# Kernel tuning notes

Hardware: AMD Instinct MI355X
Metric: run time of the kernel (lower is better)

The kernel has to match this reference:

```python
import jax, jax.numpy as jnp
import numpy as np

B, N, F, O = 4, 4096, 64, 64


def setup_inputs() -> dict:
    key = jax.random.key(0)
    k0, k1, k2, k3, k4 = jax.random.split(key, 5)
    x = jax.random.normal(k0, (B, N, F), dtype=jnp.float32)
    # adj_transform: Linear(2F -> 1): weight (2F,), bias scalar
    adj_w = jax.random.normal(k1, (2 * F,), dtype=jnp.float32) * (1.0 / np.sqrt(2 * F))
    adj_b = jax.random.normal(k2, (), dtype=jnp.float32)
    # GCN weight: xavier_normal_ over (F, O)
    weight = jax.random.normal(k3, (F, O), dtype=jnp.float32) * np.sqrt(2.0 / (F + O))
    bias = jax.random.normal(k4, (O,), dtype=jnp.float32)
    return {"x": x, "adj_w": adj_w, "adj_b": adj_b, "weight": weight, "bias": bias}


def reference(x, adj_w, adj_b, weight, bias):
    f = x.shape[-1]
    # Original: tmp[b,i,j] = x[b,j]; adj[b,i,j] = Linear(cat(x[b,j], x[b,i]))
    # = x[b,j]\u00b7adj_w[:F] + x[b,i]\u00b7adj_w[F:] + adj_b  (exact decomposition,
    # avoids materializing the (B,N,N,2F) concat tensor)
    s_col = jnp.einsum('bnf,f->bn', x, adj_w[:f])   # contributes along j
    s_row = jnp.einsum('bnf,f->bn', x, adj_w[f:])   # contributes along i
    adj = s_row[:, :, None] + s_col[:, None, :] + adj_b  # (B, N, N)
    # symmetric degree normalization with clamp(min=1)
    deg_inv_sqrt = jnp.clip(adj.sum(axis=-1), 1.0, None) ** -0.5  # (B, N)
    adj = deg_inv_sqrt[:, :, None] * adj * deg_inv_sqrt[:, None, :]
    out = jnp.einsum('bij,bjo->bio', adj, x @ weight) + bias
    return jax.nn.relu(out)
```

## Files before the change

### kernel.cpp

```cpp
#include <hip/hip_runtime.h>

#define Bq 4
#define Nq 4096
#define Fq 64
#define Oq 64


__global__ __launch_bounds__(256) void k1_rowdots(
    const float* __restrict__ x, const float* __restrict__ adj_w,
    float* __restrict__ s_row, float* __restrict__ s_col,
    float* __restrict__ blocksum) {
  int r = blockIdx.x * 256 + threadIdx.x;
  const float4* xr = reinterpret_cast<const float4*>(x + (size_t)r * Fq);
  const float4* w0 = reinterpret_cast<const float4*>(adj_w);
  const float4* w1 = reinterpret_cast<const float4*>(adj_w + Fq);
  float sc = 0.f, sr = 0.f;
#pragma unroll
  for (int k = 0; k < Fq / 4; ++k) {
    float4 v = xr[k];
    float4 a = w0[k];
    float4 b = w1[k];
    sc += v.x * a.x + v.y * a.y + v.z * a.z + v.w * a.w;
    sr += v.x * b.x + v.y * b.y + v.z * b.z + v.w * b.w;
  }
  s_col[r] = sc;
  s_row[r] = sr;
  __shared__ float red[256];
  red[threadIdx.x] = sc;
  __syncthreads();
  for (int s = 128; s > 0; s >>= 1) {
    if (threadIdx.x < s) red[threadIdx.x] += red[threadIdx.x + s];
    __syncthreads();
  }
  if (threadIdx.x == 0) blocksum[blockIdx.x] = red[0];
}

__global__ __launch_bounds__(256) void k2_weighted(
    const float* __restrict__ x, const float* __restrict__ s_row,
    const float* __restrict__ s_col, const float* __restrict__ blocksum,
    const float* __restrict__ adj_bp, float* __restrict__ pxd,
    float* __restrict__ pxsd) {
  int b = blockIdx.x >> 5;
  int chunk = blockIdx.x & 31;
  int fq = threadIdx.x & 15;
  int jsub = threadIdx.x >> 4;
  const float adj_b = adj_bp[0];
  float scs = 0.f;
#pragma unroll
  for (int k = 0; k < 16; ++k) scs += blocksum[b * 16 + k];
  const int jcnt = Nq / 32;
  int j0 = chunk * jcnt;
  float4 axd = {0.f, 0.f, 0.f, 0.f};
  float4 axsd = {0.f, 0.f, 0.f, 0.f};
  for (int j = j0 + jsub; j < j0 + jcnt; j += 16) {
    int row = b * Nq + j;
    float srj = s_row[row];
    float scj = s_col[row];
    float dj = rsqrtf(fmaxf(fmaf((float)Nq, srj + adj_b, scs), 1.0f));
    float sdj = scj * dj;
    float4 xv = reinterpret_cast<const float4*>(x + (size_t)row * Fq)[fq];
    axd.x = fmaf(dj, xv.x, axd.x);
    axd.y = fmaf(dj, xv.y, axd.y);
    axd.z = fmaf(dj, xv.z, axd.z);
    axd.w = fmaf(dj, xv.w, axd.w);
    axsd.x = fmaf(sdj, xv.x, axsd.x);
    axsd.y = fmaf(sdj, xv.y, axsd.y);
    axsd.z = fmaf(sdj, xv.z, axsd.z);
    axsd.w = fmaf(sdj, xv.w, axsd.w);
  }
  __shared__ float red[2][16][64];
  *reinterpret_cast<float4*>(&red[0][jsub][fq * 4]) = axd;
  *reinterpret_cast<float4*>(&red[1][jsub][fq * 4]) = axsd;
  __syncthreads();
  int t = threadIdx.x;
  if (t < 64) {
    float s = 0.f;
#pragma unroll
    for (int c = 0; c < 16; ++c) s += red[0][c][t];
    pxd[blockIdx.x * 64 + t] = s;
  } else if (t < 128) {
    int f = t & 63;
    float s = 0.f;
#pragma unroll
    for (int c = 0; c < 16; ++c) s += red[1][c][f];
    pxsd[blockIdx.x * 64 + f] = s;
  }
}

__global__ __launch_bounds__(256) void k3_out(
    const float* __restrict__ s_row, const float* __restrict__ blocksum,
    const float* __restrict__ adj_bp, const float* __restrict__ pxd,
    const float* __restrict__ pxsd, const float* __restrict__ weight,
    const float* __restrict__ bias, float* __restrict__ out) {
  int b = blockIdx.x >> 6;
  int ibase = (blockIdx.x & 63) << 6;
  const float adj_b = adj_bp[0];
  float scs = 0.f;
#pragma unroll
  for (int k = 0; k < 16; ++k) scs += blocksum[b * 16 + k];
  __shared__ float xdl[64], xsdl[64], u[64], v[64];
  int t = threadIdx.x;
  if (t < 128) {
    int f = t & 63;
    const float* p = ((t < 64) ? pxd : pxsd) + (size_t)(b * 32) * 64 + f;
    float a = 0.f;
#pragma unroll
    for (int c = 0; c < 32; ++c) a += p[c * 64];
    if (t < 64)
      xdl[f] = a;
    else
      xsdl[f] = a;
  }
  __syncthreads();
  if (t < 128) {
    int o = t & 63;
    const float* src = (t < 64) ? xdl : xsdl;
    float acc = 0.f;
#pragma unroll
    for (int f = 0; f < Fq; ++f) acc = fmaf(src[f], weight[f * Oq + o], acc);
    if (t < 64)
      u[o] = acc;
    else
      v[o] = acc;
  }
  __syncthreads();
  int o0 = (t & 15) * 4;
#pragma unroll
  for (int pass = 0; pass < 4; ++pass) {
    int row = ibase + pass * 16 + (t >> 4);
    int rg = b * Nq + row;
    float sr = s_row[rg];
    float rowsum = fmaf((float)Nq, sr + adj_b, scs);
    float di = rsqrtf(fmaxf(rowsum, 1.0f));
    float a = di * (sr + adj_b);
    float4 r;
    r.x = fmaxf(0.f, fmaf(a, u[o0 + 0], fmaf(di, v[o0 + 0], bias[o0 + 0])));
    r.y = fmaxf(0.f, fmaf(a, u[o0 + 1], fmaf(di, v[o0 + 1], bias[o0 + 1])));
    r.z = fmaxf(0.f, fmaf(a, u[o0 + 2], fmaf(di, v[o0 + 2], bias[o0 + 2])));
    r.w = fmaxf(0.f, fmaf(a, u[o0 + 3], fmaf(di, v[o0 + 3], bias[o0 + 3])));
    reinterpret_cast<float4*>(out + (size_t)rg * Oq)[t & 15] = r;
  }
}

extern "C" void kernel_launch(void* const* d_in, const int* in_sizes, int n_in,
                              void* d_out, int out_size, void* d_ws,
                              size_t ws_size, hipStream_t stream) {
  const float* x = (const float*)d_in[0];
  const float* adj_w = (const float*)d_in[1];
  const float* adj_b = (const float*)d_in[2];
  const float* weight = (const float*)d_in[3];
  const float* bias = (const float*)d_in[4];
  float* out = (float*)d_out;

  float* ws = (float*)d_ws;
  float* s_row = ws;
  float* s_col = ws + Bq * Nq;
  float* blocksum = ws + 2 * Bq * Nq;
  float* pxd = blocksum + 64;
  float* pxsd = pxd + 128 * 64;

  k1_rowdots<<<64, 256, 0, stream>>>(x, adj_w, s_row, s_col, blocksum);
  k2_weighted<<<Bq * 32, 256, 0, stream>>>(x, s_row, s_col, blocksum, adj_b,
                                           pxd, pxsd);
  k3_out<<<256, 256, 0, stream>>>(s_row, blocksum, adj_b, pxd, pxsd, weight,
                                  bias, out);
}
```

Before: 72.66 us.

## Fuse three kernels into one cooperative kernel with grid syncs

Merges the row-dot, weighted-sum and output kernels into a single cooperative launch of 256 blocks. Each block handles 64 rows and keeps s_row, s_col and degree values in shared memory across phases, with two grid-wide syncs replacing the kernel boundaries. This removes two launch gaps and the global round-trips for per-row scalars. In exchange it depends on all blocks being co-resident and adds the cost of the grid barriers.

```diff
diff --git a/kernel.cpp b/kernel.cpp
--- a/kernel.cpp
+++ b/kernel.cpp
@@ -1,111 +1,125 @@
 #include <hip/hip_runtime.h>
+#include <hip/hip_cooperative_groups.h>
+
+namespace cg = cooperative_groups;
 
 #define Bq 4
 #define Nq 4096
 #define Fq 64
 #define Oq 64
 
+__global__ __launch_bounds__(256) void gcn_fused(
+    const float* __restrict__ x, const float* __restrict__ adj_w,
+    const float* __restrict__ adj_bp, const float* __restrict__ weight,
+    const float* __restrict__ bias, float* __restrict__ out,
+    float* __restrict__ blksum, float* __restrict__ pxd,
+    float* __restrict__ pxsd) {
+  const int t = threadIdx.x;
+  const int blk = blockIdx.x;
+  const int batch = blk >> 6;
+  const float adj_b = adj_bp[0];
 
-__global__ __launch_bounds__(256) void k1_rowdots(
-    const float* __restrict__ x, const float* __restrict__ adj_w,
-    float* __restrict__ s_row, float* __restrict__ s_col,
-    float* __restrict__ blocksum) {
-  int r = blockIdx.x * 256 + threadIdx.x;
-  const float4* xr = reinterpret_cast<const float4*>(x + (size_t)r * Fq);
-  const float4* w0 = reinterpret_cast<const float4*>(adj_w);
-  const float4* w1 = reinterpret_cast<const float4*>(adj_w + Fq);
-  float sc = 0.f, sr = 0.f;
+  __shared__ float ls_row[64], ls_col[64], ld[64], lsd[64];
+  __shared__ float red[2][16][64];
+  __shared__ float xdl[64], xsdl[64], ul[64], vl[64];
+  __shared__ float s_scs;
+
+  {
+    const int g = t >> 2;
+    const int l = t & 3;
+    const int r = blk * 64 + g;
+    const float4* xr = reinterpret_cast<const float4*>(x + (size_t)r * Fq);
+    const float4* w0 = reinterpret_cast<const float4*>(adj_w);
+    const float4* w1 = reinterpret_cast<const float4*>(adj_w + Fq);
+    float sc = 0.f, sr = 0.f;
 #pragma unroll
-  for (int k = 0; k < Fq / 4; ++k) {
-    float4 v = xr[k];
-    float4 a = w0[k];
-    float4 b = w1[k];
-    sc += v.x * a.x + v.y * a.y + v.z * a.z + v.w * a.w;
-    sr += v.x * b.x + v.y * b.y + v.z * b.z + v.w * b.w;
+    for (int k = 0; k < 4; ++k) {
+      const int idx = k * 4 + l;
+      float4 xv = xr[idx];
+      float4 wa = w0[idx];
+      float4 wb = w1[idx];
+      sc += xv.x * wa.x + xv.y * wa.y + xv.z * wa.z + xv.w * wa.w;
+      sr += xv.x * wb.x + xv.y * wb.y + xv.z * wb.z + xv.w * wb.w;
+    }
+    sc += __shfl_xor(sc, 1);
+    sc += __shfl_xor(sc, 2);
+    sr += __shfl_xor(sr, 1);
+    sr += __shfl_xor(sr, 2);
+    if (l == 0) {
+      ls_col[g] = sc;
+      ls_row[g] = sr;
+    }
   }
-  s_col[r] = sc;
-  s_row[r] = sr;
-  __shared__ float red[256];
-  red[threadIdx.x] = sc;
   __syncthreads();
-  for (int s = 128; s > 0; s >>= 1) {
-    if (threadIdx.x < s) red[threadIdx.x] += red[threadIdx.x + s];
-    __syncthreads();
+  if (t < 64) {
+    float val = ls_col[t];
+#pragma unroll
+    for (int m = 1; m < 64; m <<= 1) val += __shfl_xor(val, m);
+    if (t == 0) blksum[blk] = val;
   }
-  if (threadIdx.x == 0) blocksum[blockIdx.x] = red[0];
-}
+  __threadfence();
+  cg::this_grid().sync();
 
-__global__ __launch_bounds__(256) void k2_weighted(
-    const float* __restrict__ x, const float* __restrict__ s_row,
-    const float* __restrict__ s_col, const float* __restrict__ blocksum,
-    const float* __restrict__ adj_bp, float* __restrict__ pxd,
-    float* __restrict__ pxsd) {
-  int b = blockIdx.x >> 5;
-  int chunk = blockIdx.x & 31;
-  int fq = threadIdx.x & 15;
-  int jsub = threadIdx.x >> 4;
-  const float adj_b = adj_bp[0];
-  float scs = 0.f;
+  if (t < 64) {
+    float val = blksum[batch * 64 + t];
 #pragma unroll
-  for (int k = 0; k < 16; ++k) scs += blocksum[b * 16 + k];
-  const int jcnt = Nq / 32;
-  int j0 = chunk * jcnt;
-  float4 axd = {0.f, 0.f, 0.f, 0.f};
-  float4 axsd = {0.f, 0.f, 0.f, 0.f};
-  for (int j = j0 + jsub; j < j0 + jcnt; j += 16) {
-    int row = b * Nq + j;
-    float srj = s_row[row];
-    float scj = s_col[row];
-    float dj = rsqrtf(fmaxf(fmaf((float)Nq, srj + adj_b, scs), 1.0f));
-    float sdj = scj * dj;
-    float4 xv = reinterpret_cast<const float4*>(x + (size_t)row * Fq)[fq];
-    axd.x = fmaf(dj, xv.x, axd.x);
-    axd.y = fmaf(dj, xv.y, axd.y);
-    axd.z = fmaf(dj, xv.z, axd.z);
-    axd.w = fmaf(dj, xv.w, axd.w);
-    axsd.x = fmaf(sdj, xv.x, axsd.x);
-    axsd.y = fmaf(sdj, xv.y, axsd.y);
-    axsd.z = fmaf(sdj, xv.z, axsd.z);
-    axsd.w = fmaf(sdj, xv.w, axsd.w);
+    for (int m = 1; m < 64; m <<= 1) val += __shfl_xor(val, m);
+    if (t == 0) s_scs = val;
   }
-  __shared__ float red[2][16][64];
-  *reinterpret_cast<float4*>(&red[0][jsub][fq * 4]) = axd;
-  *reinterpret_cast<float4*>(&red[1][jsub][fq * 4]) = axsd;
   __syncthreads();
-  int t = threadIdx.x;
+  const float scs = s_scs;
+  if (t < 64) {
+    float dg = rsqrtf(fmaxf(fmaf((float)Nq, ls_row[t] + adj_b, scs), 1.0f));
+    ld[t] = dg;
+    lsd[t] = ls_col[t] * dg;
+  }
+  __syncthreads();
+  {
+    const int fq = t & 15;
+    const int jsub = t >> 4;
+    const float4* x4 =
+        reinterpret_cast<const float4*>(x) + (size_t)blk * 64 * 16 + fq;
+    float4 axd = {0.f, 0.f, 0.f, 0.f};
+    float4 axsd = {0.f, 0.f, 0.f, 0.f};
+#pragma unroll
+    for (int j = jsub; j < 64; j += 16) {
+      const float dj = ld[j];
+      const float sdj = lsd[j];
+      float4 xv = x4[j * 16];
+      axd.x = fmaf(dj, xv.x, axd.x);
+      axd.y = fmaf(dj, xv.y, axd.y);
+      axd.z = fmaf(dj, xv.z, axd.z);
+      axd.w = fmaf(dj, xv.w, axd.w);
+      axsd.x = fmaf(sdj, xv.x, axsd.x);
+      axsd.y = fmaf(sdj, xv.y, axsd.y);
+      axsd.z = fmaf(sdj, xv.z, axsd.z);
+      axsd.w = fmaf(sdj, xv.w, axsd.w);
+    }
+    *reinterpret_cast<float4*>(&red[0][jsub][fq * 4]) = axd;
+    *reinterpret_cast<float4*>(&red[1][jsub][fq * 4]) = axsd;
+  }
+  __syncthreads();
   if (t < 64) {
     float s = 0.f;
 #pragma unroll
     for (int c = 0; c < 16; ++c) s += red[0][c][t];
-    pxd[blockIdx.x * 64 + t] = s;
+    pxd[blk * 64 + t] = s;
   } else if (t < 128) {
-    int f = t & 63;
+    const int f = t & 63;
     float s = 0.f;
 #pragma unroll
     for (int c = 0; c < 16; ++c) s += red[1][c][f];
-    pxsd[blockIdx.x * 64 + f] = s;
+    pxsd[blk * 64 + f] = s;
   }
-}
+  __threadfence();
+  cg::this_grid().sync();
 
-__global__ __launch_bounds__(256) void k3_out(
-    const float* __restrict__ s_row, const float* __restrict__ blocksum,
-    const float* __restrict__ adj_bp, const float* __restrict__ pxd,
-    const float* __restrict__ pxsd, const float* __restrict__ weight,
-    const float* __restrict__ bias, float* __restrict__ out) {
-  int b = blockIdx.x >> 6;
-  int ibase = (blockIdx.x & 63) << 6;
-  const float adj_b = adj_bp[0];
-  float scs = 0.f;
-#pragma unroll
-  for (int k = 0; k < 16; ++k) scs += blocksum[b * 16 + k];
-  __shared__ float xdl[64], xsdl[64], u[64], v[64];
-  int t = threadIdx.x;
   if (t < 128) {
-    int f = t & 63;
-    const float* p = ((t < 64) ? pxd : pxsd) + (size_t)(b * 32) * 64 + f;
+    const int f = t & 63;
+    const float* p = ((t < 64) ? pxd : pxsd) + (size_t)batch * 64 * 64 + f;
     float a = 0.f;
 #pragma unroll
-    for (int c = 0; c < 32; ++c) a += p[c * 64];
+    for (int c = 0; c < 64; ++c) a += p[c * 64];
     if (t < 64)
       xdl[f] = a;
     else
@@ -113,32 +127,34 @@
   }
   __syncthreads();
   if (t < 128) {
-    int o = t & 63;
+    const int o = t & 63;
     const float* src = (t < 64) ? xdl : xsdl;
     float acc = 0.f;
 #pragma unroll
     for (int f = 0; f < Fq; ++f) acc = fmaf(src[f], weight[f * Oq + o], acc);
     if (t < 64)
-      u[o] = acc;
+      ul[o] = acc;
     else
-      v[o] = acc;
+      vl[o] = acc;
   }
   __syncthreads();
-  int o0 = (t & 15) * 4;
+  {
+    const int oq = t & 15;
+    const int o0 = oq * 4;
+    const float4 bv = reinterpret_cast<const float4*>(bias)[oq];
 #pragma unroll
-  for (int pass = 0; pass < 4; ++pass) {
-    int row = ibase + pass * 16 + (t >> 4);
-    int rg = b * Nq + row;
-    float sr = s_row[rg];
-    float rowsum = fmaf((float)Nq, sr + adj_b, scs);
-    float di = rsqrtf(fmaxf(rowsum, 1.0f));
-    float a = di * (sr + adj_b);
-    float4 r;
-    r.x = fmaxf(0.f, fmaf(a, u[o0 + 0], fmaf(di, v[o0 + 0], bias[o0 + 0])));
-    r.y = fmaxf(0.f, fmaf(a, u[o0 + 1], fmaf(di, v[o0 + 1], bias[o0 + 1])));
-    r.z = fmaxf(0.f, fmaf(a, u[o0 + 2], fmaf(di, v[o0 + 2], bias[o0 + 2])));
-    r.w = fmaxf(0.f, fmaf(a, u[o0 + 3], fmaf(di, v[o0 + 3], bias[o0 + 3])));
-    reinterpret_cast<float4*>(out + (size_t)rg * Oq)[t & 15] = r;
+    for (int pass = 0; pass < 4; ++pass) {
+      const int g = pass * 16 + (t >> 4);
+      const int r = blk * 64 + g;
+      const float di = ld[g];
+      const float a = di * (ls_row[g] + adj_b);
+      float4 rr;
+      rr.x = fmaxf(0.f, fmaf(a, ul[o0 + 0], fmaf(di, vl[o0 + 0], bv.x)));
+      rr.y = fmaxf(0.f, fmaf(a, ul[o0 + 1], fmaf(di, vl[o0 + 1], bv.y)));
+      rr.z = fmaxf(0.f, fmaf(a, ul[o0 + 2], fmaf(di, vl[o0 + 2], bv.z)));
+      rr.w = fmaxf(0.f, fmaf(a, ul[o0 + 3], fmaf(di, vl[o0 + 3], bv.w)));
+      reinterpret_cast<float4*>(out + (size_t)r * Oq)[oq] = rr;
+    }
   }
 }
 
@@ -153,15 +169,13 @@
   float* out = (float*)d_out;
 
   float* ws = (float*)d_ws;
-  float* s_row = ws;
-  float* s_col = ws + Bq * Nq;
-  float* blocksum = ws + 2 * Bq * Nq;
-  float* pxd = blocksum + 64;
-  float* pxsd = pxd + 128 * 64;
+  float* blksum = ws;
+  float* pxd = ws + 256;
+  float* pxsd = pxd + 256 * 64;
 
-  k1_rowdots<<<64, 256, 0, stream>>>(x, adj_w, s_row, s_col, blocksum);
-  k2_weighted<<<Bq * 32, 256, 0, stream>>>(x, s_row, s_col, blocksum, adj_b,
-                                           pxd, pxsd);
-  k3_out<<<256, 256, 0, stream>>>(s_row, blocksum, adj_b, pxd, pxsd, weight,
-                                  bias, out);
+  void* args[] = {(void*)&x,   (void*)&adj_w,  (void*)&adj_b,
+                  (void*)&weight, (void*)&bias, (void*)&out,
+                  (void*)&blksum, (void*)&pxd,  (void*)&pxsd};
+  hipLaunchCooperativeKernel((void*)gcn_fused, dim3(256), dim3(256), args, 0,
+                             stream);
 }
```

New measurement: 161.1 us. 2.22x slower.
